# Optimization experiments

Measured on AMD Instinct MI355X. Metric: run time of the kernel, lower is better.

The kernel has to match this reference:

```python
import jax, jax.numpy as jnp
import numpy as np

N, P, Q, H_DIM, HEADS, D = 4096, 128, 128, 256, 8, 64  # D = graph_dim // heads


def setup_inputs() -> dict:
    key = jax.random.key(0)
    ks = jax.random.split(key, 6)
    s = 0.05  # small scale to keep tanh/softmax in a sane range
    return {
        "x_prices": jax.random.normal(ks[0], (N, P), jnp.float32),
        "x_news": jax.random.normal(ks[1], (N, Q), jnp.float32),
        "W_bil": jax.random.normal(ks[2], (H_DIM, P, Q), jnp.float32) * s,
        "b_bil": jax.random.normal(ks[3], (H_DIM,), jnp.float32) * s,
        "Wt": jax.random.normal(ks[4], (HEADS, D, H_DIM), jnp.float32) * s,
        "a_vec": jax.random.normal(ks[5], (HEADS, 2 * D), jnp.float32) * s,
    }


def reference(x_prices, x_news, W_bil, b_bil, Wt, a_vec):
    # nn.Bilinear: out[n,h] = sum_pq x_prices[n,p] W[h,p,q] x_news[n,q] + b[h]
    x = jnp.einsum('np,hpq,nq->nh', x_prices, W_bil, x_news) + b_bil  # (N, hidden)

    # Per-head linear transform: fc_transform (no bias). Wt: (heads, d, hidden)
    xt = jnp.einsum('nh,kdh->knd', x, Wt)  # (heads, N, d)

    # Attention score a . [x_i, x_j] split into src/dst halves -> broadcast add
    d = Wt.shape[1]
    a_src, a_dst = a_vec[:, :d], a_vec[:, d:]
    s_src = jnp.einsum('knd,kd->kn', xt, a_src)  # (heads, N)
    s_dst = jnp.einsum('knd,kd->kn', xt, a_dst)  # (heads, N)
    scores = s_src[:, :, None] + s_dst[:, None, :]  # (heads, N, N)
    scores = jnp.where(scores >= 0, scores, 0.2 * scores)  # LeakyReLU(0.2)

    attn = jax.nn.softmax(scores, axis=-1)  # softmax over neighbors j
    out = jnp.einsum('knm,kmd->knd', attn, xt)  # (heads, N, d)

    # Concatenate head outputs on feature dim, then tanh
    out = jnp.transpose(out, (1, 0, 2)).reshape(xt.shape[1], -1)  # (N, heads*d)
    return jnp.tanh(out)
```

## Files before the change

### kernel.cpp

```cpp
#include <hip/hip_runtime.h>
#include <hip/hip_bf16.h>

typedef unsigned short ushort;
typedef unsigned int uint;
typedef unsigned long long u64;
typedef _Float16 f16;

#define NN 4096
#define PP 128
#define QQ 128
#define HD 256
#define KH 8
#define DD 64
#define KK 16384

typedef _Float16 f16x2 __attribute__((ext_vector_type(2)));
typedef _Float16 f16x4 __attribute__((ext_vector_type(4)));
typedef _Float16 f16x8 __attribute__((ext_vector_type(8)));
typedef __fp16 fp16x2 __attribute__((ext_vector_type(2)));
typedef float f32x4 __attribute__((ext_vector_type(4)));

__device__ inline void async_lds16(const void* g, void* l) {
  __builtin_amdgcn_global_load_lds(
      (const __attribute__((address_space(1))) unsigned int*)g,
      (__attribute__((address_space(3))) unsigned int*)l, 16, 0, 0);
}

__global__ __launch_bounds__(256) void k0_split2(
    const float* __restrict__ W, const float* __restrict__ Wt,
    f16* __restrict__ hiW, f16* __restrict__ loW,
    f16* __restrict__ hiT, f16* __restrict__ loT, float* __restrict__ xz) {
  const int tid = blockIdx.x * 256 + threadIdx.x;
  const int i = tid * 4;
  if (tid < (NN * HD) / 4)
    *(float4*)&xz[i] = make_float4(0.f, 0.f, 0.f, 0.f);
  const float* src;
  f16 *hi, *lo;
  int off;
  if (i < HD * PP * QQ) { src = W; hi = hiW; lo = loW; off = i; }
  else { src = Wt; hi = hiT; lo = loT; off = i - HD * PP * QQ; }
  const float4 w = *(const float4*)&src[off];
  const float wf[4] = {w.x, w.y, w.z, w.w};
  f16x4 hv, lv;
#pragma unroll
  for (int j = 0; j < 4; ++j) {
    const f16 h = (f16)wf[j];
    hv[j] = h;
    lv[j] = (f16)(wf[j] - (float)h);
  }
  *(f16x4*)&hi[off] = hv;
  *(f16x4*)&lo[off] = lv;
}

__global__ __launch_bounds__(256, 4) void k1_bilinear(
    const float* __restrict__ xp, const float* __restrict__ xn,
    const f16* __restrict__ Whi, const f16* __restrict__ Wlo,
    float* __restrict__ xout) {
  __shared__ f16 whi[128 * 32];
  __shared__ f16 wlo[128 * 32];
  __shared__ f16 zhi[128 * 40];
  __shared__ float xpt[8][128];

  const int t = threadIdx.x;
  const int bid = blockIdx.x;
  const int xcd = bid & 7, slot = bid >> 3;
  const int jpan = slot >> 5, n_idx = slot & 31;
  const int pan = xcd + 8 * jpan;
  const int n0 = n_idx * 128;
  const int kb = (pan & 15) * (KK / 16);
  const int h0 = (pan >> 4) * 128;
  const int pb = kb >> 7;

  for (int idx = t; idx < 1024; idx += 256) {
    const int p = idx & 7, n = idx >> 3;
    xpt[p][n] = xp[(size_t)(n0 + n) * PP + pb + p];
  }

  const int l = t & 63, w = t >> 6;
  const int wr = (w >> 1) * 64, wc = (w & 1) * 64;

  int aoff[4], boff[4];
#pragma unroll
  for (int i = 0; i < 4; ++i)
    aoff[i] = (wr + i * 16 + (l & 15)) * 40 + (l >> 4) * 8;
#pragma unroll
  for (int j = 0; j < 4; ++j) {
    const int hr = wc + j * 16 + (l & 15);
    boff[j] = hr * 32 + (((l >> 4) ^ ((hr ^ (hr >> 2)) & 3)) * 8);
  }

  const int shb = t >> 2, seg = t & 3;
  int gsw[2];
#pragma unroll
  for (int g = 0; g < 2; ++g) {
    const int r = shb + 64 * g;
    gsw[g] = seg ^ ((r ^ (r >> 2)) & 3);
  }

  const int zn = t >> 1, zko = (t & 1) * 16;

  f32x4 acc[4][4];
#pragma unroll
  for (int i = 0; i < 4; ++i)
#pragma unroll
    for (int j = 0; j < 4; ++j) acc[i][j] = (f32x4)0.f;

  for (int c = 0; c < 32; ++c) {
    const int kc = kb + c * 32;
    const int pl = c >> 2;
    const int q0 = (c & 3) * 32;

    __syncthreads();

#pragma unroll
    for (int g = 0; g < 2; ++g) {
      const int r = shb + 64 * g;
      async_lds16(Whi + (size_t)(h0 + r) * KK + kc + gsw[g] * 8,
                  whi + r * 32 + seg * 8);
      async_lds16(Wlo + (size_t)(h0 + r) * KK + kc + gsw[g] * 8,
                  wlo + r * 32 + seg * 8);
    }

    {
      const float xpv = xpt[pl][zn];
      const float* xr = xn + (size_t)(n0 + zn) * QQ + q0 + zko;
      const float4 v0 = ((const float4*)xr)[0];
      const float4 v1 = ((const float4*)xr)[1];
      const float4 v2 = ((const float4*)xr)[2];
      const float4 v3 = ((const float4*)xr)[3];
      float zz[16] = {v0.x, v0.y, v0.z, v0.w, v1.x, v1.y, v1.z, v1.w,
                      v2.x, v2.y, v2.z, v2.w, v3.x, v3.y, v3.z, v3.w};
      union { uint u[8]; uint4 q[2]; } ph;
#pragma unroll
      for (int j = 0; j < 8; ++j) {
        union { fp16x2 h; uint u; } cv;
        cv.h = __builtin_amdgcn_cvt_pkrtz(xpv * zz[2 * j], xpv * zz[2 * j + 1]);
        ph.u[j] = cv.u;
      }
      const int zo = zn * 40 + zko;
      *(uint4*)&zhi[zo] = ph.q[0];
      *(uint4*)&zhi[zo + 8] = ph.q[1];
    }

    __syncthreads();

    f16x8 Ah[4];
#pragma unroll
    for (int i = 0; i < 4; ++i) Ah[i] = *(const f16x8*)&zhi[aoff[i]];
#pragma unroll
    for (int j = 0; j < 4; ++j) {
      const f16x8 Bh = *(const f16x8*)&whi[boff[j]];
      const f16x8 Bl = *(const f16x8*)&wlo[boff[j]];
#pragma unroll
      for (int i = 0; i < 4; ++i)
        acc[i][j] = __builtin_amdgcn_mfma_f32_16x16x32_f16(Ah[i], Bh, acc[i][j], 0, 0, 0);
#pragma unroll
      for (int i = 0; i < 4; ++i)
        acc[i][j] = __builtin_amdgcn_mfma_f32_16x16x32_f16(Ah[i], Bl, acc[i][j], 0, 0, 0);
    }
  }

#pragma unroll
  for (int i = 0; i < 4; ++i)
#pragma unroll
    for (int j = 0; j < 4; ++j) {
      const int row = n0 + wr + i * 16 + (l >> 4) * 4;
      const int col = h0 + wc + j * 16 + (l & 15);
#pragma unroll
      for (int r = 0; r < 4; ++r)
        atomicAdd(&xout[(size_t)(row + r) * HD + col], acc[i][j][r]);
    }
}

__global__ __launch_bounds__(256) void k23_xt(
    const float* __restrict__ x, const float* __restrict__ bb,
    const f16* __restrict__ Wthi, const f16* __restrict__ Wtlo,
    const float* __restrict__ av, float* __restrict__ xt,
    float* __restrict__ ssrc, float* __restrict__ sdst) {
  __shared__ f16 ah[64 * 40];
  __shared__ f16 bh[128 * 32];
  __shared__ f16 bl[128 * 32];
  __shared__ float red1[2][64][17];
  __shared__ float red2[2][64][17];
  const int t = threadIdx.x;
  const int n0 = blockIdx.x * 64;
  const int c0 = blockIdx.y * 128;
  const int l = t & 63, w = t >> 6;
  const int wn = (w & 1) * 32, wcc = (w >> 1) * 64;

  int aoff[2], boff[4];
#pragma unroll
  for (int i = 0; i < 2; ++i)
    aoff[i] = (wn + i * 16 + (l & 15)) * 40 + (l >> 4) * 8;
#pragma unroll
  for (int j = 0; j < 4; ++j) {
    const int hr = wcc + j * 16 + (l & 15);
    boff[j] = hr * 32 + (((l >> 4) ^ ((hr ^ (hr >> 2)) & 3)) * 8);
  }

  f32x4 acc[2][4];
#pragma unroll
  for (int i = 0; i < 2; ++i)
#pragma unroll
    for (int j = 0; j < 4; ++j) acc[i][j] = (f32x4)0.f;

  for (int kc = 0; kc < HD; kc += 32) {
    __syncthreads();
    {
      const int row = t >> 2, sg = t & 3;
      const float* xr = &x[(size_t)(n0 + row) * HD + kc + sg * 8];
      const float4 xa = ((const float4*)xr)[0];
      const float4 xb = ((const float4*)xr)[1];
      const float4 ba = *(const float4*)&bb[kc + sg * 8];
      const float4 bv = *(const float4*)&bb[kc + sg * 8 + 4];
      f16x8 o;
      o[0] = (f16)(xa.x + ba.x); o[1] = (f16)(xa.y + ba.y);
      o[2] = (f16)(xa.z + ba.z); o[3] = (f16)(xa.w + ba.w);
      o[4] = (f16)(xb.x + bv.x); o[5] = (f16)(xb.y + bv.y);
      o[6] = (f16)(xb.z + bv.z); o[7] = (f16)(xb.w + bv.w);
      *(f16x8*)&ah[row * 40 + sg * 8] = o;
    }
#pragma unroll
    for (int g = 0; g < 2; ++g) {
      const int slot = g * 256 + t;
      const int col = slot >> 2, ps = slot & 3;
      const int ls = ps ^ ((col ^ (col >> 2)) & 3);
      *(uint4*)&bh[col * 32 + ps * 8] =
          *(const uint4*)&Wthi[(size_t)(c0 + col) * HD + kc + ls * 8];
      *(uint4*)&bl[col * 32 + ps * 8] =
          *(const uint4*)&Wtlo[(size_t)(c0 + col) * HD + kc + ls * 8];
    }
    __syncthreads();
    f16x8 Af[2];
#pragma unroll
    for (int i = 0; i < 2; ++i) Af[i] = *(const f16x8*)&ah[aoff[i]];
#pragma unroll
    for (int j = 0; j < 4; ++j) {
      const f16x8 Bh = *(const f16x8*)&bh[boff[j]];
      const f16x8 Bl = *(const f16x8*)&bl[boff[j]];
#pragma unroll
      for (int i = 0; i < 2; ++i)
        acc[i][j] = __builtin_amdgcn_mfma_f32_16x16x32_f16(Af[i], Bh, acc[i][j], 0, 0, 0);
#pragma unroll
      for (int i = 0; i < 2; ++i)
        acc[i][j] = __builtin_amdgcn_mfma_f32_16x16x32_f16(Af[i], Bl, acc[i][j], 0, 0, 0);
    }
  }

  const int hh = w >> 1;
  const int khead = (c0 >> 6) + hh;
  float a1v[4], a2v[4];
#pragma unroll
  for (int j = 0; j < 4; ++j) {
    const int d = j * 16 + (l & 15);
    a1v[j] = av[khead * (2 * DD) + d];
    a2v[j] = av[khead * (2 * DD) + DD + d];
  }

#pragma unroll
  for (int i = 0; i < 2; ++i)
#pragma unroll
    for (int r = 0; r < 4; ++r) {
      const int rowl = wn + i * 16 + (l >> 4) * 4 + r;
      float p1 = 0.f, p2 = 0.f;
#pragma unroll
      for (int j = 0; j < 4; ++j) {
        p1 += acc[i][j][r] * a1v[j];
        p2 += acc[i][j][r] * a2v[j];
      }
      red1[hh][rowl][l & 15] = p1;
      red2[hh][rowl][l & 15] = p2;
    }

#pragma unroll
  for (int i = 0; i < 2; ++i)
#pragma unroll
    for (int j = 0; j < 4; ++j) {
      const int row = n0 + wn + i * 16 + (l >> 4) * 4;
      const int colg = c0 + wcc + j * 16 + (l & 15);
      const int k = colg >> 6, d = colg & 63;
#pragma unroll
      for (int r = 0; r < 4; ++r)
        xt[((size_t)(k * NN + row + r)) * DD + d] = acc[i][j][r];
    }

  __syncthreads();
  {
    const int hh2 = t >> 7;
    const int which = (t >> 6) & 1;
    const int row = t & 63;
    const float* rp = which ? &red2[hh2][row][0] : &red1[hh2][row][0];
    float s = 0.f;
#pragma unroll
    for (int g = 0; g < 16; ++g) s += rp[g];
    const int kk = (c0 >> 6) + hh2;
    if (which) sdst[kk * NN + n0 + row] = s;
    else ssrc[kk * NN + n0 + row] = s;
  }
}

__global__ __launch_bounds__(256) void k4_rank(
    const float* __restrict__ sdst, float* __restrict__ vsorted,
    int* __restrict__ perm) {
  __shared__ u64 kv[4096];
  __shared__ ushort pcnt[256];
  const int k = blockIdx.y, t = threadIdx.x;
  for (int i = t; i < 4096; i += 256) {
    const uint u = __float_as_uint(sdst[k * NN + i]);
    const uint key = (u & 0x80000000u) ? ~u : (u | 0x80000000u);
    kv[i] = ((u64)key << 32) | (uint)i;
  }
  __syncthreads();
  const int idx = t & 127;
  const int half = t >> 7;
  const u64 my = kv[blockIdx.x * 128 + idx];
  const int j0 = half * 2048;
  int cnt = 0;
#pragma unroll 16
  for (int j = 0; j < 2048; ++j) cnt += (kv[j0 + j] < my) ? 1 : 0;
  pcnt[t] = (ushort)cnt;
  __syncthreads();
  if (t < 128) {
    const int tot = (int)pcnt[t] + (int)pcnt[t + 128];
    const u64 my2 = kv[blockIdx.x * 128 + t];
    const uint key = (uint)(my2 >> 32);
    const uint u = (key & 0x80000000u) ? (key ^ 0x80000000u) : ~key;
    vsorted[k * NN + tot] = __uint_as_float(u);
    perm[k * NN + tot] = (int)(my2 & 0xFFFFFFFFu);
  }
}

__global__ __launch_bounds__(64) void k4b_chunksum(
    const float* __restrict__ vs, const int* __restrict__ perm,
    const float* __restrict__ xt, float* __restrict__ Chi, float* __restrict__ Clo) {
  __shared__ float rows[64][64];
  __shared__ float eh[64], el[64];
  const int c = blockIdx.x, k = blockIdx.y, t = threadIdx.x;
  const int base = k * NN + c * 64;
  {
    const float v = vs[base + t];
    eh[t] = __expf(v);
    el[t] = __expf(0.2f * v);
  }
#pragma unroll
  for (int r = 0; r < 16; ++r) {
    const int i = r * 4 + (t >> 4);
    const int p = perm[base + i];
    *(float4*)&rows[i][(t & 15) * 4] =
        *(const float4*)&xt[((size_t)(k * NN + p)) * DD + (t & 15) * 4];
  }
  __syncthreads();
  float shi = 0.f, slo = 0.f, whs = 0.f, wls = 0.f;
#pragma unroll 8
  for (int i = 0; i < 64; ++i) {
    const float val = rows[i][t];
    shi += eh[i] * val; slo += el[i] * val;
    whs += eh[i]; wls += el[i];
  }
  const int cb = (k * 64 + c) * 65;
  Chi[cb + t] = shi;
  Clo[cb + t] = slo;
  if (t == 0) { Chi[cb + 64] = whs; Clo[cb + 64] = wls; }
}

__global__ __launch_bounds__(64) void k4d_expand(
    const float* __restrict__ vs, const int* __restrict__ perm,
    const float* __restrict__ xt, const float* __restrict__ Chi,
    const float* __restrict__ Clo, float* __restrict__ Phi,
    float* __restrict__ Plo) {
  __shared__ float schi[64 * 65];
  __shared__ float sclo[64 * 65];
  __shared__ float rows[64][64];
  __shared__ float eh[64], el[64];
  const int c = blockIdx.x, k = blockIdx.y, t = threadIdx.x;
  const int base = k * NN + c * 64;
  for (int idx = t; idx < 4160; idx += 64) {
    schi[idx] = Chi[k * 4160 + idx];
    sclo[idx] = Clo[k * 4160 + idx];
  }
  {
    const float v = vs[base + t];
    eh[t] = __expf(v);
    el[t] = __expf(0.2f * v);
  }
#pragma unroll
  for (int r = 0; r < 16; ++r) {
    const int i = r * 4 + (t >> 4);
    const int p = perm[base + i];
    *(float4*)&rows[i][(t & 15) * 4] =
        *(const float4*)&xt[((size_t)(k * NN + p)) * DD + (t & 15) * 4];
  }
  __syncthreads();

  float run = 0.f, wrun = 0.f;
  for (int cc = 0; cc < c; ++cc) {
    run += sclo[cc * 65 + t];
    wrun += sclo[cc * 65 + 64];
  }
  float runS = 0.f, wrunS = 0.f;
  for (int cc = c + 1; cc < 64; ++cc) {
    runS += schi[cc * 65 + t];
    wrunS += schi[cc * 65 + 64];
  }

  for (int i = 0; i < 64; ++i) {
    const size_t rb = ((size_t)(k * 4097) + c * 64 + i) * 65;
    Plo[rb + t] = run;
    if (t == 0) Plo[rb + 64] = wrun;
    run += el[i] * rows[i][t];
    wrun += el[i];
  }
  if (c == 63) {
    const size_t rb = ((size_t)(k * 4097) + 4096) * 65;
    Plo[rb + t] = run;
    if (t == 0) Plo[rb + 64] = wrun;
  }
  for (int i = 63; i >= 0; --i) {
    runS += eh[i] * rows[i][t];
    wrunS += eh[i];
    const size_t rb = ((size_t)(k * 4097) + c * 64 + i) * 65;
    Phi[rb + t] = runS;
    if (t == 0) Phi[rb + 64] = wrunS;
  }
  if (c == 63) {
    const size_t rb = ((size_t)(k * 4097) + 4096) * 65;
    Phi[rb + t] = 0.f;
    if (t == 0) Phi[rb + 64] = 0.f;
  }
}

__global__ __launch_bounds__(256) void k6_final(
    const float* __restrict__ ssrc, const float* __restrict__ vsorted,
    const float* __restrict__ Phi, const float* __restrict__ Plo,
    float* __restrict__ out) {
  __shared__ float vsh[4096];
  __shared__ int posSh[16];
  const int t = threadIdx.x;
  const int q0 = blockIdx.x * 16;
  const int k = q0 >> 12;
  for (int idx = t; idx < 1024; idx += 256)
    *(float4*)&vsh[idx * 4] = *(const float4*)&vsorted[k * NN + idx * 4];
  __syncthreads();
  if (t < 16) {
    const float thr = -ssrc[q0 + t];
    int lo = 0, hi = 4096;
    while (lo < hi) {
      const int mid = (lo + hi) >> 1;
      if (vsh[mid] < thr) lo = mid + 1; else hi = mid;
    }
    posSh[t] = lo;
  }
  __syncthreads();
  const int d = t & 63;
#pragma unroll
  for (int qq = 0; qq < 4; ++qq) {
    const int ql = qq * 4 + (t >> 6);
    const int qi = q0 + ql;
    const int n = qi & 4095;
    const float u = ssrc[qi];
    const size_t rb = ((size_t)(k * 4097) + posSh[ql]) * 65;
    const float eu = __expf(u), el = __expf(0.2f * u);
    const float num = eu * Phi[rb + d] + el * Plo[rb + d];
    const float den = eu * Phi[rb + 64] + el * Plo[rb + 64];
    out[(size_t)n * (KH * DD) + k * DD + d] = tanhf(num / den);
  }
}

extern "C" void kernel_launch(void* const* d_in, const int* in_sizes, int n_in,
                              void* d_out, int out_size, void* d_ws, size_t ws_size,
                              hipStream_t stream) {
  const float* xp = (const float*)d_in[0];
  const float* xn = (const float*)d_in[1];
  const float* W = (const float*)d_in[2];
  const float* bb = (const float*)d_in[3];
  const float* Wt = (const float*)d_in[4];
  const float* av = (const float*)d_in[5];
  float* out = (float*)d_out;

  char* ws = (char*)d_ws;
  f16* Whi    = (f16*)(ws);
  f16* Wlo    = (f16*)(ws + 8388608);
  float* Phi  = (float*)(ws);
  float* Plo  = (float*)(ws + 8522240);
  float* x    = (float*)(ws + 17044480);
  float* xt   = (float*)(ws + 21238784);
  f16* Wthi   = (f16*)(ws + 31724544);
  f16* Wtlo   = (f16*)(ws + 31986688);
  float* ssrc = (float*)(ws + 32248832);
  float* sdst = (float*)(ws + 32379904);
  float* vsort= (float*)(ws + 32510976);
  int*   perm = (int*)  (ws + 32642048);
  float* Chi  = (float*)(ws + 32773120);
  float* Clo  = (float*)(ws + 32906240);

  k0_split2<<<(HD * PP * QQ + KH * DD * HD) / 1024, 256, 0, stream>>>(
      W, Wt, Whi, Wlo, Wthi, Wtlo, x);
  k1_bilinear<<<1024, 256, 0, stream>>>(xp, xn, Whi, Wlo, x);
  k23_xt<<<dim3(NN / 64, 4), 256, 0, stream>>>(x, bb, Wthi, Wtlo, av, xt, ssrc, sdst);
  k4_rank<<<dim3(32, KH), 256, 0, stream>>>(sdst, vsort, perm);
  k4b_chunksum<<<dim3(64, KH), 64, 0, stream>>>(vsort, perm, xt, Chi, Clo);
  k4d_expand<<<dim3(64, KH), 64, 0, stream>>>(vsort, perm, xt, Chi, Clo, Phi, Plo);
  k6_final<<<(KH * NN) / 16, 256, 0, stream>>>(ssrc, vsort, Phi, Plo, out);
}
```

Baseline: 253.2 us.

## Swizzle A-tile LDS layout, prefetch news rows, split expand kernel passes

Replaces the padded (stride 40) LDS layout of the A operand in the bilinear and xt kernels with an XOR-swizzled stride-32 layout, cutting LDS use while trying to keep reads free of bank conflicts. The bilinear kernel also loads the next chunk of x_news into registers right after the barrier so the global load overlaps the MFMA work. The expand kernel is split along a new grid z dimension so the forward and backward prefix passes run as separate blocks, doubling parallelism and halving per-block LDS. The cost is extra register pressure from the prefetch and a duplicated gather of rows per pass.

```diff
diff --git a/kernel.cpp b/kernel.cpp
--- a/kernel.cpp
+++ b/kernel.cpp
@@ -58,7 +58,7 @@
     float* __restrict__ xout) {
   __shared__ f16 whi[128 * 32];
   __shared__ f16 wlo[128 * 32];
-  __shared__ f16 zhi[128 * 40];
+  __shared__ f16 zhi[128 * 32];
   __shared__ float xpt[8][128];
 
   const int t = threadIdx.x;
@@ -81,8 +81,10 @@
 
   int aoff[4], boff[4];
 #pragma unroll
-  for (int i = 0; i < 4; ++i)
-    aoff[i] = (wr + i * 16 + (l & 15)) * 40 + (l >> 4) * 8;
+  for (int i = 0; i < 4; ++i) {
+    const int row = wr + i * 16 + (l & 15);
+    aoff[i] = row * 32 + (((l >> 4) ^ ((row ^ (row >> 2)) & 3)) * 8);
+  }
 #pragma unroll
   for (int j = 0; j < 4; ++j) {
     const int hr = wc + j * 16 + (l & 15);
@@ -98,17 +100,26 @@
   }
 
   const int zn = t >> 1, zko = (t & 1) * 16;
+  const int zm = (zn ^ (zn >> 2)) & 3;
+  const int zs0 = (t & 1) * 2;
+  const int zo0 = zn * 32 + ((zs0 ^ zm) * 8);
+  const int zo1 = zn * 32 + (((zs0 + 1) ^ zm) * 8);
 
   f32x4 acc[4][4];
 #pragma unroll
   for (int i = 0; i < 4; ++i)
 #pragma unroll
     for (int j = 0; j < 4; ++j) acc[i][j] = (f32x4)0.f;
+
+  const float* xr0 = xn + (size_t)(n0 + zn) * QQ + zko;
+  float4 xv0 = ((const float4*)xr0)[0];
+  float4 xv1 = ((const float4*)xr0)[1];
+  float4 xv2 = ((const float4*)xr0)[2];
+  float4 xv3 = ((const float4*)xr0)[3];
 
   for (int c = 0; c < 32; ++c) {
     const int kc = kb + c * 32;
     const int pl = c >> 2;
-    const int q0 = (c & 3) * 32;
 
     __syncthreads();
 
@@ -123,13 +134,8 @@
 
     {
       const float xpv = xpt[pl][zn];
-      const float* xr = xn + (size_t)(n0 + zn) * QQ + q0 + zko;
-      const float4 v0 = ((const float4*)xr)[0];
-      const float4 v1 = ((const float4*)xr)[1];
-      const float4 v2 = ((const float4*)xr)[2];
-      const float4 v3 = ((const float4*)xr)[3];
-      float zz[16] = {v0.x, v0.y, v0.z, v0.w, v1.x, v1.y, v1.z, v1.w,
-                      v2.x, v2.y, v2.z, v2.w, v3.x, v3.y, v3.z, v3.w};
+      float zz[16] = {xv0.x, xv0.y, xv0.z, xv0.w, xv1.x, xv1.y, xv1.z, xv1.w,
+                      xv2.x, xv2.y, xv2.z, xv2.w, xv3.x, xv3.y, xv3.z, xv3.w};
       union { uint u[8]; uint4 q[2]; } ph;
 #pragma unroll
       for (int j = 0; j < 8; ++j) {
@@ -137,12 +143,20 @@
         cv.h = __builtin_amdgcn_cvt_pkrtz(xpv * zz[2 * j], xpv * zz[2 * j + 1]);
         ph.u[j] = cv.u;
       }
-      const int zo = zn * 40 + zko;
-      *(uint4*)&zhi[zo] = ph.q[0];
-      *(uint4*)&zhi[zo + 8] = ph.q[1];
+      *(uint4*)&zhi[zo0] = ph.q[0];
+      *(uint4*)&zhi[zo1] = ph.q[1];
     }
 
     __syncthreads();
+
+    if (c < 31) {
+      const int q0n = ((c + 1) & 3) * 32;
+      const float* xr = xn + (size_t)(n0 + zn) * QQ + q0n + zko;
+      xv0 = ((const float4*)xr)[0];
+      xv1 = ((const float4*)xr)[1];
+      xv2 = ((const float4*)xr)[2];
+      xv3 = ((const float4*)xr)[3];
+    }
 
     f16x8 Ah[4];
 #pragma unroll
@@ -177,7 +191,7 @@
     const f16* __restrict__ Wthi, const f16* __restrict__ Wtlo,
     const float* __restrict__ av, float* __restrict__ xt,
     float* __restrict__ ssrc, float* __restrict__ sdst) {
-  __shared__ f16 ah[64 * 40];
+  __shared__ f16 ah[64 * 32];
   __shared__ f16 bh[128 * 32];
   __shared__ f16 bl[128 * 32];
   __shared__ float red1[2][64][17];
@@ -190,8 +204,10 @@
 
   int aoff[2], boff[4];
 #pragma unroll
-  for (int i = 0; i < 2; ++i)
-    aoff[i] = (wn + i * 16 + (l & 15)) * 40 + (l >> 4) * 8;
+  for (int i = 0; i < 2; ++i) {
+    const int row = wn + i * 16 + (l & 15);
+    aoff[i] = row * 32 + (((l >> 4) ^ ((row ^ (row >> 2)) & 3)) * 8);
+  }
 #pragma unroll
   for (int j = 0; j < 4; ++j) {
     const int hr = wcc + j * 16 + (l & 15);
@@ -218,7 +234,8 @@
       o[2] = (f16)(xa.z + ba.z); o[3] = (f16)(xa.w + ba.w);
       o[4] = (f16)(xb.x + bv.x); o[5] = (f16)(xb.y + bv.y);
       o[6] = (f16)(xb.z + bv.z); o[7] = (f16)(xb.w + bv.w);
-      *(f16x8*)&ah[row * 40 + sg * 8] = o;
+      const int sgs = sg ^ ((row ^ (row >> 2)) & 3);
+      *(f16x8*)&ah[row * 32 + sgs * 8] = o;
     }
 #pragma unroll
     for (int g = 0; g < 2; ++g) {
@@ -368,20 +385,17 @@
     const float* __restrict__ xt, const float* __restrict__ Chi,
     const float* __restrict__ Clo, float* __restrict__ Phi,
     float* __restrict__ Plo) {
-  __shared__ float schi[64 * 65];
-  __shared__ float sclo[64 * 65];
+  __shared__ float scs[64 * 65];
   __shared__ float rows[64][64];
-  __shared__ float eh[64], el[64];
+  __shared__ float ev[64];
   const int c = blockIdx.x, k = blockIdx.y, t = threadIdx.x;
+  const int pass = blockIdx.z;
   const int base = k * NN + c * 64;
-  for (int idx = t; idx < 4160; idx += 64) {
-    schi[idx] = Chi[k * 4160 + idx];
-    sclo[idx] = Clo[k * 4160 + idx];
-  }
+  const float* Cs = pass ? Chi : Clo;
+  for (int idx = t; idx < 4160; idx += 64) scs[idx] = Cs[k * 4160 + idx];
   {
     const float v = vs[base + t];
-    eh[t] = __expf(v);
-    el[t] = __expf(0.2f * v);
+    ev[t] = pass ? __expf(v) : __expf(0.2f * v);
   }
 #pragma unroll
   for (int r = 0; r < 16; ++r) {
@@ -392,40 +406,42 @@
   }
   __syncthreads();
 
-  float run = 0.f, wrun = 0.f;
-  for (int cc = 0; cc < c; ++cc) {
-    run += sclo[cc * 65 + t];
-    wrun += sclo[cc * 65 + 64];
-  }
-  float runS = 0.f, wrunS = 0.f;
-  for (int cc = c + 1; cc < 64; ++cc) {
-    runS += schi[cc * 65 + t];
-    wrunS += schi[cc * 65 + 64];
-  }
-
-  for (int i = 0; i < 64; ++i) {
-    const size_t rb = ((size_t)(k * 4097) + c * 64 + i) * 65;
-    Plo[rb + t] = run;
-    if (t == 0) Plo[rb + 64] = wrun;
-    run += el[i] * rows[i][t];
-    wrun += el[i];
-  }
-  if (c == 63) {
-    const size_t rb = ((size_t)(k * 4097) + 4096) * 65;
-    Plo[rb + t] = run;
-    if (t == 0) Plo[rb + 64] = wrun;
-  }
-  for (int i = 63; i >= 0; --i) {
-    runS += eh[i] * rows[i][t];
-    wrunS += eh[i];
-    const size_t rb = ((size_t)(k * 4097) + c * 64 + i) * 65;
-    Phi[rb + t] = runS;
-    if (t == 0) Phi[rb + 64] = wrunS;
-  }
-  if (c == 63) {
-    const size_t rb = ((size_t)(k * 4097) + 4096) * 65;
-    Phi[rb + t] = 0.f;
-    if (t == 0) Phi[rb + 64] = 0.f;
+  if (pass == 0) {
+    float run = 0.f, wrun = 0.f;
+    for (int cc = 0; cc < c; ++cc) {
+      run += scs[cc * 65 + t];
+      wrun += scs[cc * 65 + 64];
+    }
+    for (int i = 0; i < 64; ++i) {
+      const size_t rb = ((size_t)(k * 4097) + c * 64 + i) * 65;
+      Plo[rb + t] = run;
+      if (t == 0) Plo[rb + 64] = wrun;
+      run += ev[i] * rows[i][t];
+      wrun += ev[i];
+    }
+    if (c == 63) {
+      const size_t rb = ((size_t)(k * 4097) + 4096) * 65;
+      Plo[rb + t] = run;
+      if (t == 0) Plo[rb + 64] = wrun;
+    }
+  } else {
+    float runS = 0.f, wrunS = 0.f;
+    for (int cc = c + 1; cc < 64; ++cc) {
+      runS += scs[cc * 65 + t];
+      wrunS += scs[cc * 65 + 64];
+    }
+    for (int i = 63; i >= 0; --i) {
+      runS += ev[i] * rows[i][t];
+      wrunS += ev[i];
+      const size_t rb = ((size_t)(k * 4097) + c * 64 + i) * 65;
+      Phi[rb + t] = runS;
+      if (t == 0) Phi[rb + 64] = wrunS;
+    }
+    if (c == 63) {
+      const size_t rb = ((size_t)(k * 4097) + 4096) * 65;
+      Phi[rb + t] = 0.f;
+      if (t == 0) Phi[rb + 64] = 0.f;
+    }
   }
 }
 
@@ -499,6 +515,6 @@
   k23_xt<<<dim3(NN / 64, 4), 256, 0, stream>>>(x, bb, Wthi, Wtlo, av, xt, ssrc, sdst);
   k4_rank<<<dim3(32, KH), 256, 0, stream>>>(sdst, vsort, perm);
   k4b_chunksum<<<dim3(64, KH), 64, 0, stream>>>(vsort, perm, xt, Chi, Clo);
-  k4d_expand<<<dim3(64, KH), 64, 0, stream>>>(vsort, perm, xt, Chi, Clo, Phi, Plo);
+  k4d_expand<<<dim3(64, KH, 2), 64, 0, stream>>>(vsort, perm, xt, Chi, Clo, Phi, Plo);
   k6_final<<<(KH * NN) / 16, 256, 0, stream>>>(ssrc, vsort, Phi, Plo, out);
 }
```

Measured after the change: 246.7 us. 1.03x faster.
